# Optimization experiments

Measured on AMD Instinct MI355X. Metric: run time of the kernel, lower is better.

Reference implementation:

```python
import jax, jax.numpy as jnp
import numpy as np

N = 2048; E = 65536; T = 6; F_IN = 2
H_ENC = 256; LAT = 128; H_DEC = 256
PRED = 6
MIN_X, MAX_X = 0.0, 1.0
MIN_Y, MAX_Y = 0.0, 1.0
MIN_EW, MAX_EW = 0.0, 0.5
VISUAL_RANGE = 0.5


def setup_inputs() -> dict:
    key = jax.random.key(0)
    ks = jax.random.split(key, 17)
    p = lambda k, shape: jax.random.normal(k, shape, jnp.float32) * 0.05
    return {
        "x_seq": jax.random.uniform(ks[0], (T, N, F_IN), jnp.float32),
        "edge_index_seq": jax.random.randint(ks[1], (T, 2, E), 0, N),
        "edge_weight_seq": jax.random.uniform(ks[2], (T, E), jnp.float32, 1e-3, 1.0),
        "h_enc": jnp.zeros((N, H_ENC), jnp.float32),
        "h_dec": jnp.zeros((N, H_DEC), jnp.float32),
        "enc_Wx": p(ks[3], (3, 2, F_IN, H_ENC)),
        "enc_bx": p(ks[4], (3, H_ENC)),
        "enc_Wh": p(ks[5], (3, 2, H_ENC, H_ENC)),
        "enc_bh": p(ks[6], (3, H_ENC)),
        "enc_lin_W": p(ks[7], (H_ENC, LAT)),
        "enc_lin_b": p(ks[8], (LAT,)),
        "dec_Wx": p(ks[9], (3, 2, LAT, H_DEC)),
        "dec_bx": p(ks[10], (3, H_DEC)),
        "dec_Wh": p(ks[11], (3, 2, H_DEC, H_DEC)),
        "dec_bh": p(ks[12], (3, H_DEC)),
        "dec_lin_W": p(ks[13], (H_DEC, F_IN)),
        "dec_lin_b": p(ks[14], (F_IN,)),
    }


def _sparse_conv_fn(edge_index, edge_weight, n):
    # ChebConv K=2, sym normalization, lambda_max=2 => T1(L_hat) = -D^-1/2 A D^-1/2
    src, dst = edge_index[0], edge_index[1]
    deg = jax.ops.segment_sum(edge_weight, src, num_segments=n)
    dinv = jnp.where(deg > 0, jax.lax.rsqrt(jnp.where(deg > 0, deg, 1.0)), 0.0)
    norm = -dinv[src] * edge_weight * dinv[dst]  # [E]

    def conv(x, W, b):  # W: [2, in, out]
        tx1 = jax.ops.segment_sum(norm[:, None] * x[src], dst, num_segments=n)
        return x @ W[0] + tx1 @ W[1] + b
    return conv


def _dense_conv_fn(y_hat):
    # graph rebuilt from detached predicted coords (radius graph, dense masked form)
    c = jax.lax.stop_gradient(y_hat)
    px = c[:, 0] * (MAX_X - MIN_X) + MIN_X
    py = c[:, 1] * (MAX_Y - MIN_Y) + MIN_Y
    coords = jnp.stack((px, py), axis=1)  # [N, 2]
    d = jnp.linalg.norm(coords[:, None, :] - coords[None, :, :], axis=2)  # [N, N]
    mask = (d < VISUAL_RANGE) & (d > 0)
    w = jnp.where(mask, (d - MIN_EW) / (MAX_EW - MIN_EW), 0.0)
    deg = w.sum(axis=1)
    dinv = jnp.where(deg > 0, jax.lax.rsqrt(jnp.where(deg > 0, deg, 1.0)), 0.0)
    M = -(dinv[:, None] * w) * dinv[None, :]  # scaled-Laplacian off-diagonal

    def conv(x, W, b):
        return x @ W[0] + (M @ x) @ W[1] + b
    return conv


def _gru(conv, x, H, Wx, bx, Wh, bh):
    # GConvGRU gates: each gate = conv_x(X) + conv_h(H)
    z = jax.nn.sigmoid(conv(x, Wx[0], bx[0]) + conv(H, Wh[0], bh[0]))
    r = jax.nn.sigmoid(conv(x, Wx[1], bx[1]) + conv(H, Wh[1], bh[1]))
    h_tilde = jnp.tanh(conv(x, Wx[2], bx[2]) + conv(H * r, Wh[2], bh[2]))
    return z * H + (1.0 - z) * h_tilde


def reference(x_seq, edge_index_seq, edge_weight_seq, h_enc, h_dec,
              enc_Wx, enc_bx, enc_Wh, enc_bh, enc_lin_W, enc_lin_b,
              dec_Wx, dec_bx, dec_Wh, dec_bh, dec_lin_W, dec_lin_b):
    n = x_seq.shape[1]

    def step(conv, x, he, hd):
        he0 = _gru(conv, x, he, enc_Wx, enc_bx, enc_Wh, enc_bh)
        z = jax.nn.relu(he0) @ enc_lin_W + enc_lin_b
        hd0 = _gru(conv, z, hd, dec_Wx, dec_bx, dec_Wh, dec_bh)
        y_hat = jax.nn.relu(hd0) @ dec_lin_W + dec_lin_b
        return y_hat, he0, hd0

    # observed snapshots (sparse edge-list graphs)
    for t in range(x_seq.shape[0]):
        conv = _sparse_conv_fn(edge_index_seq[t], edge_weight_seq[t], n)
        y_hat, h_enc, h_dec = step(conv, x_seq[t], h_enc, h_dec)

    preds = [y_hat]
    for _ in range(PRED - 1):
        conv = _dense_conv_fn(y_hat)
        y_hat, h_enc, h_dec = step(conv, y_hat, h_enc, h_dec)
        preds.append(y_hat)
    return jnp.stack(preds)  # [PRED, N, 2]
```

## Files before the change

### kernel.cpp

```cpp
#include <hip/hip_runtime.h>
#include <math.h>

#define NN 2048
#define EE 65536
#define T_OBS 6
#define FIN 2
#define HE 256
#define LT 128
#define PREDN 6
#define DMM_NZ 8
#define ZR_NZ 4
#define GT_NZ 8
#define LIN_NZ 8

typedef __attribute__((ext_vector_type(8))) short short8v;
typedef __attribute__((ext_vector_type(4))) float float4v;

static __device__ __forceinline__ unsigned short f2bf(float f) {
    union { float f; unsigned u; } v; v.f = f;
    unsigned r = v.u + 0x7fff + ((v.u >> 16) & 1);
    return (unsigned short)(r >> 16);
}

static __device__ __forceinline__ void bfsplit(float f, unsigned short& h,
                                               unsigned short& l) {
    unsigned u = __float_as_uint(f);
    h = (unsigned short)(u >> 16);
    float hf = __uint_as_float(u & 0xffff0000u);
    l = (unsigned short)(__float_as_uint(f - hf) >> 16);
}

__global__ void k_degcnt(const int* __restrict__ src, const int* __restrict__ dst,
                         const float* __restrict__ ew,
                         float* __restrict__ deg, int* __restrict__ cnt) {
    int e = blockIdx.x * blockDim.x + threadIdx.x;
    if (e < EE) {
        atomicAdd(&deg[src[e]], ew[e]);
        atomicAdd(&cnt[dst[e]], 1);
    }
}

__global__ void k_scan(const int* __restrict__ cnt, const float* __restrict__ deg,
                       int* __restrict__ roff, int* __restrict__ cur,
                       float* __restrict__ dinv) {
    __shared__ int part[256];
    int t = threadIdx.x;
#pragma unroll
    for (int i = t; i < NN; i += 256) {
        float d = deg[i];
        dinv[i] = d > 0.f ? 1.f / sqrtf(d) : 0.f;
    }
    int loc[8];
// ... 15 lines not shown
        roff[idx] = run;
        cur[idx] = run;
        run += loc[i];
    }
    if (t == 255) roff[NN] = run;
}

__global__ void k_scatter2(const int* __restrict__ src, const int* __restrict__ dst,
                           const float* __restrict__ ew, const float* __restrict__ dinv,
                           int* __restrict__ cur,
                           int* __restrict__ csr_src, float* __restrict__ csr_nrm) {
    int e = blockIdx.x * blockDim.x + threadIdx.x;
    if (e < EE) {
        int s = src[e], d = dst[e];
        int p = atomicAdd(&cur[d], 1);
        csr_src[p] = s;
        csr_nrm[p] = -dinv[s] * ew[e] * dinv[d];
    }
}

template <int F>
__global__ void k_spmm_v(const int* __restrict__ roff, const int* __restrict__ csr_src,
                         const float* __restrict__ csr_nrm,
                         const float* __restrict__ X, float* __restrict__ out) {
    int w = threadIdx.x >> 6, lane = threadIdx.x & 63;
    int nid = (blockIdx.x << 2) + w;
    int c = lane << 2;
    int s0 = roff[nid], s1 = roff[nid + 1];
    float4 acc = make_float4(0.f, 0.f, 0.f, 0.f);
    int s = s0;
    for (; s + 8 <= s1; s += 8) {
        int is[8]; float ws[8];
#pragma unroll
        for (int j = 0; j < 8; j++) { is[j] = csr_src[s + j]; ws[j] = csr_nrm[s + j]; }
        if (c < F) {
            float4 xv[8];
#pragma unroll
            for (int j = 0; j < 8; j++) xv[j] = *(const float4*)&X[(size_t)is[j] * F + c];
#pragma unroll
            for (int j = 0; j < 8; j++) {
                acc.x = fmaf(ws[j], xv[j].x, acc.x);
                acc.y = fmaf(ws[j], xv[j].y, acc.y);
                acc.z = fmaf(ws[j], xv[j].z, acc.z);
                acc.w = fmaf(ws[j], xv[j].w, acc.w);
            }
        }
    }
    for (; s < s1; ++s) {
        int i0 = csr_src[s]; float w0 = csr_nrm[s];
        if (c < F) {
            float4 xv = *(const float4*)&X[(size_t)i0 * F + c];
            acc.x = fmaf(w0, xv.x, acc.x);
            acc.y = fmaf(w0, xv.y, acc.y);
            acc.z = fmaf(w0, xv.z, acc.z);
            acc.w = fmaf(w0, xv.w, acc.w);
        }
    }
    if (c < F) *(float4*)&out[(size_t)nid * F + c] = acc;
}

__global__ void k_spmm2(const int* __restrict__ roff, const int* __restrict__ csr_src,
                        const float* __restrict__ csr_nrm,
                        const float* __restrict__ X, float* __restrict__ out) {
    int nid = blockIdx.x * blockDim.x + threadIdx.x;
    if (nid < NN) {
        int s0 = roff[nid], s1 = roff[nid + 1];
        float a0 = 0.f, a1 = 0.f;
        for (int s = s0; s < s1; ++s) {
            int i = csr_src[s]; float w = csr_nrm[s];
            float2 xv = *(const float2*)&X[2 * i];
            a0 = fmaf(w, xv.x, a0);
            a1 = fmaf(w, xv.y, a1);
        }
        out[2 * nid] = a0;
        out[2 * nid + 1] = a1;
    }
}

__global__ void k_ddeg(const float* __restrict__ c, float* __restrict__ dinv) {
    int i = blockIdx.x;
    int t = threadIdx.x;
    float xi = c[2 * i], yi = c[2 * i + 1];
    float s = 0.f;
    for (int j = t; j < NN; j += 256) {
        float dx = xi - c[2 * j], dy = yi - c[2 * j + 1];
        float d = sqrtf(dx * dx + dy * dy);
        if (d > 0.f && d < 0.5f) s += 2.f * d;
    }
    __shared__ float red[256];
    red[t] = s;
    __syncthreads();
    for (int off = 128; off > 0; off >>= 1) {
        if (t < off) red[t] += red[t + off];
        __syncthreads();
    }
    if (t == 0) {
        float d = red[0];
        dinv[i] = d > 0.f ? 1.f / sqrtf(d) : 0.f;
    }
}

__global__ void k_dM(const float* __restrict__ c, const float* __restrict__ dinv,
                     float* __restrict__ M, unsigned short* __restrict__ Mb) {
    int idx = blockIdx.x * blockDim.x + threadIdx.x;
    int i = idx >> 11, j = idx & (NN - 1);
    float dx = c[2 * i] - c[2 * j], dy = c[2 * i + 1] - c[2 * j + 1];
    float d = sqrtf(dx * dx + dy * dy);
    float w = (d > 0.f && d < 0.5f) ? 2.f * d : 0.f;
    float v = -(dinv[i] * w) * dinv[j];
    M[idx] = v;
    Mb[idx] = f2bf(v);
}

template <int F>
__global__ __launch_bounds__(256) void k_dmm_mf(
    const unsigned short* __restrict__ Mb, const float* __restrict__ X,
    float* __restrict__ pbuf)
{
    __shared__ __align__(16) unsigned short Ms[64][72];
    __shared__ __align__(16) unsigned short Xs[64][72];
    const int tid = threadIdx.x;
    const int wid = tid >> 6, lane = tid & 63;
    const int m0 = blockIdx.x << 6, n0 = blockIdx.y << 6;
    const int kb0 = blockIdx.z << 8;
    const int lr = lane & 15;
    const int kg = lane >> 4;
    float4v acc[4];
#pragma unroll
    for (int t = 0; t < 4; t++) acc[t] = (float4v){0.f, 0.f, 0.f, 0.f};

    for (int kb = kb0; kb < kb0 + 256; kb += 64) {
#pragma unroll
        for (int it = 0; it < 2; it++) {
            int i = tid + it * 256;
// ... 21 lines not shown
        __syncthreads();
#pragma unroll
        for (int kh = 0; kh < 2; kh++) {
            int kk = kh * 32 + kg * 8;
            short8v a = *(const short8v*)&Ms[(wid << 4) + lr][kk];
#pragma unroll
            for (int t = 0; t < 4; t++) {
                short8v b = *(const short8v*)&Xs[(t << 4) + lr][kk];
                acc[t] = __builtin_amdgcn_mfma_f32_16x16x32_bf16(a, b, acc[t], 0, 0, 0);
            }
        }
        __syncthreads();
    }
    float* p = pbuf + (size_t)blockIdx.z * NN * F;
#pragma unroll
    for (int t = 0; t < 4; t++)
#pragma unroll
        for (int j = 0; j < 4; j++)
            p[(size_t)(m0 + (wid << 4) + (kg << 2) + j) * F + n0 + (t << 4) + lr] =
                acc[t][j];
}

template <int F, int NZ>
__global__ void k_redks(const float* __restrict__ pbuf, float* __restrict__ out) {
    const int TOT = NN * F / 4;
    int i = blockIdx.x * blockDim.x + threadIdx.x;
    if (i < TOT) {
        const float4* p = (const float4*)pbuf;
        float4 s = p[i];
#pragma unroll
        for (int z = 1; z < NZ; z++) {
            float4 v = p[(size_t)z * TOT + i];
            s.x += v.x; s.y += v.y; s.z += v.z; s.w += v.w;
        }
        ((float4*)out)[i] = s;
    }
}

__global__ void k_dmv2(const float* __restrict__ M, const float* __restrict__ X,
                       float* __restrict__ out) {
    int i = blockIdx.x;
    int t = threadIdx.x;
    float a0 = 0.f, a1 = 0.f;
    for (int j = t; j < NN; j += 256) {
        float m = M[i * NN + j];
        a0 = fmaf(m, X[2 * j], a0);
        a1 = fmaf(m, X[2 * j + 1], a1);
    }
    __shared__ float r0[256], r1[256];
    r0[t] = a0;
    r1[t] = a1;
    __syncthreads();
    for (int off = 128; off > 0; off >>= 1) {
        if (t < off) { r0[t] += r0[t + off]; r1[t] += r1[t + off]; }
        __syncthreads();
    }
    if (t == 0) { out[2 * i] = r0[0]; out[2 * i + 1] = r1[0]; }
}

template <bool RELU>
__device__ __forceinline__ void mfma_seg(
    unsigned short (*Ah)[40], unsigned short (*Al)[40],
    unsigned short (*Bh)[40], unsigned short (*Bl)[40],
    const float* __restrict__ A, int lda,
    const float* __restrict__ B, int ldb, int K,
    int m0, int tid, int wid, int lr, int kg, float4v (&acc)[4])
{
    for (int k0 = 0; k0 < K; k0 += 32) {
        {
            int r = tid >> 2, k8 = (tid & 3) << 3;
            const float* ap = &A[(size_t)(m0 + r) * lda + k0 + k8];
            float4 va = *(const float4*)ap;
            float4 vb = *(const float4*)(ap + 4);
            float v[8] = {va.x, va.y, va.z, va.w, vb.x, vb.y, vb.z, vb.w};
            short8v hv, lv;
#pragma unroll
            for (int j = 0; j < 8; j++) {
                float f = RELU ? fmaxf(v[j], 0.f) : v[j];
                unsigned short h, l;
                bfsplit(f, h, l);
                hv[j] = (short)h; lv[j] = (short)l;
            }
            *(short8v*)&Ah[r][k8] = hv;
            *(short8v*)&Al[r][k8] = lv;
        }
        {
            int k2 = (tid & 15) << 1;
            int n4 = (tid >> 4) << 2;
            const float* bp = &B[(size_t)(k0 + k2) * ldb + n4];
            float4 va = *(const float4*)bp;
            float4 vb = *(const float4*)(bp + ldb);
            float v0[4] = {va.x, va.y, va.z, va.w};
            float v1[4] = {vb.x, vb.y, vb.z, vb.w};
#pragma unroll
            for (int j = 0; j < 4; j++) {
                unsigned short h0, l0, h1, l1;
                bfsplit(v0[j], h0, l0);
                bfsplit(v1[j], h1, l1);
                *(unsigned*)&Bh[n4 + j][k2] = (unsigned)h0 | ((unsigned)h1 << 16);
                *(unsigned*)&Bl[n4 + j][k2] = (unsigned)l0 | ((unsigned)l1 << 16);
            }
        }
        __syncthreads();
        short8v ah = *(short8v*)&Ah[(wid << 4) + lr][kg << 3];
        short8v al = *(short8v*)&Al[(wid << 4) + lr][kg << 3];
#pragma unroll
        for (int t = 0; t < 4; t++) {
            short8v bh = *(short8v*)&Bh[(t << 4) + lr][kg << 3];
            short8v bl = *(short8v*)&Bl[(t << 4) + lr][kg << 3];
            acc[t] = __builtin_amdgcn_mfma_f32_16x16x32_bf16(ah, bh, acc[t], 0, 0, 0);
            acc[t] = __builtin_amdgcn_mfma_f32_16x16x32_bf16(ah, bl, acc[t], 0, 0, 0);
            acc[t] = __builtin_amdgcn_mfma_f32_16x16x32_bf16(al, bh, acc[t], 0, 0, 0);
        }
        __syncthreads();
    }
}

__global__ __launch_bounds__(256) void k_zr_ks(
    const float* __restrict__ A0, int K01, const float* __restrict__ A1,
    const float* __restrict__ H, const float* __restrict__ A3,
    const float* __restrict__ Wx, const float* __restrict__ Wh,
    float* __restrict__ pbuf)
{
    __shared__ __align__(16) unsigned short Ah[64][40], Al[64][40],
                                            Bh[64][40], Bl[64][40];
    int tid = threadIdx.x;
    int wid = tid >> 6, lane = tid & 63, lr = lane & 15, kg = lane >> 4;
    int m0 = blockIdx.x << 6;
    int g = blockIdx.y >> 2;
    int n0 = (blockIdx.y & 3) << 6;
    float4v acc[4];
#pragma unroll
    for (int t = 0; t < 4; t++) acc[t] = (float4v){0.f, 0.f, 0.f, 0.f};
    const float* As[4] = {A0, A1, H, A3};
    const int ldas[4] = {K01, K01, HE, HE};
    const float* Bs[4] = {
        Wx + (size_t)(g * 2 + 0) * K01 * HE + n0,
        Wx + (size_t)(g * 2 + 1) * K01 * HE + n0,
        Wh + (size_t)(g * 2 + 0) * HE * HE + n0,
        Wh + (size_t)(g * 2 + 1) * HE * HE + n0};
    const int Ks[4] = {K01, K01, HE, HE};
    int chunk = (2 * K01 + 2 * HE) / ZR_NZ;
    int lo = blockIdx.z * chunk, hi = lo + chunk;
    int off = 0;
#pragma unroll
    for (int s = 0; s < 4; s++) {
        int a = lo - off; a = a < 0 ? 0 : a;
        int b = hi - off; b = b > Ks[s] ? Ks[s] : b;
        if (b > a)
            mfma_seg<false>(Ah, Al, Bh, Bl, As[s] + a, ldas[s],
                            Bs[s] + (size_t)a * HE, HE, b - a,
                            m0, tid, wid, lr, kg, acc);
        off += Ks[s];
    }
    float* p = pbuf + (size_t)blockIdx.z * NN * 512;
    int cbase = (g << 8) + n0;
#pragma unroll
    for (int t = 0; t < 4; t++)
#pragma unroll
        for (int j = 0; j < 4; j++)
            p[(size_t)(m0 + (wid << 4) + (kg << 2) + j) * 512 + cbase + (t << 4) + lr] =
                acc[t][j];
}

__global__ void k_zr_ep(const float* __restrict__ pbuf,
                        const float* __restrict__ bx, const float* __restrict__ bh,
                        const float* __restrict__ H,
                        const float* __restrict__ x2, const float* __restrict__ ax2,
                        const float* __restrict__ Wx,
                        float* __restrict__ gz, float* __restrict__ hr)
{
    int i = blockIdx.x * 256 + threadIdx.x;
    const float4* p = (const float4*)pbuf;
    const size_t S = (size_t)NN * 512 / 4;
    float4 a = p[i];
#pragma unroll
    for (int z = 1; z < ZR_NZ; z++) {
        float4 v = p[(size_t)z * S + i];
        a.x += v.x; a.y += v.y; a.z += v.z; a.w += v.w;
    }
    int row = i >> 7, c = (i & 127) << 2;
    int g = c >> 8, cc = c & 255;
    if (Wx) {
        float x0 = x2[2 * row], x1 = x2[2 * row + 1];
        float q0 = ax2[2 * row], q1 = ax2[2 * row + 1];
        const float* W0 = Wx + (size_t)(g * 2 + 0) * FIN * HE;
        const float* W1 = Wx + (size_t)(g * 2 + 1) * FIN * HE;
        float4 w00 = *(const float4*)&W0[cc];
        float4 w01 = *(const float4*)&W0[HE + cc];
        float4 w10 = *(const float4*)&W1[cc];
        float4 w11 = *(const float4*)&W1[HE + cc];
        a.x += x0 * w00.x + x1 * w01.x + q0 * w10.x + q1 * w11.x;
        a.y += x0 * w00.y + x1 * w01.y + q0 * w10.y + q1 * w11.y;
        a.z += x0 * w00.z + x1 * w01.z + q0 * w10.z + q1 * w11.z;
        a.w += x0 * w00.w + x1 * w01.w + q0 * w10.w + q1 * w11.w;
    }
    float4 b0 = *(const float4*)&bx[c];
    float4 b1 = *(const float4*)&bh[c];
    float4 s;
    s.x = 1.f / (1.f + expf(-(a.x + b0.x + b1.x)));
    s.y = 1.f / (1.f + expf(-(a.y + b0.y + b1.y)));
    s.z = 1.f / (1.f + expf(-(a.z + b0.z + b1.z)));
    s.w = 1.f / (1.f + expf(-(a.w + b0.w + b1.w)));
    if (c < HE) {
        *(float4*)&gz[(size_t)row * HE + c] = s;
    } else {
        float4 h = *(const float4*)&H[(size_t)row * HE + cc];
        s.x *= h.x; s.y *= h.y; s.z *= h.z; s.w *= h.w;
        *(float4*)&hr[(size_t)row * HE + cc] = s;
    }
}

__global__ __launch_bounds__(256) void k_gt_ks(
    const float* __restrict__ A0, int K01, const float* __restrict__ A1,
    const float* __restrict__ hr, const float* __restrict__ A3,
    const float* __restrict__ Wx2, const float* __restrict__ Wh2,
    float* __restrict__ pbuf)
{
    __shared__ __align__(16) unsigned short Ah[64][40], Al[64][40],
                                            Bh[64][40], Bl[64][40];
    int tid = threadIdx.x;
    int wid = tid >> 6, lane = tid & 63, lr = lane & 15, kg = lane >> 4;
    int m0 = blockIdx.x << 6;
    int n0 = blockIdx.y << 6;
    float4v acc[4];
#pragma unroll
    for (int t = 0; t < 4; t++) acc[t] = (float4v){0.f, 0.f, 0.f, 0.f};
    const float* As[4] = {A0, A1, hr, A3};
    const int ldas[4] = {K01, K01, HE, HE};
    const float* Bs[4] = {
        Wx2 + n0,
        Wx2 + (size_t)K01 * HE + n0,
        Wh2 + n0,
        Wh2 + (size_t)HE * HE + n0};
    const int Ks[4] = {K01, K01, HE, HE};
    int chunk = (2 * K01 + 2 * HE) / GT_NZ;
    int lo = blockIdx.z * chunk, hi = lo + chunk;
    int off = 0;
#pragma unroll
    for (int s = 0; s < 4; s++) {
        int a = lo - off; a = a < 0 ? 0 : a;
        int b = hi - off; b = b > Ks[s] ? Ks[s] : b;
        if (b > a)
            mfma_seg<false>(Ah, Al, Bh, Bl, As[s] + a, ldas[s],
                            Bs[s] + (size_t)a * HE, HE, b - a,
                            m0, tid, wid, lr, kg, acc);
        off += Ks[s];
    }
    float* p = pbuf + (size_t)blockIdx.z * NN * HE;
#pragma unroll
    for (int t = 0; t < 4; t++)
#pragma unroll
        for (int j = 0; j < 4; j++)
            p[(size_t)(m0 + (wid << 4) + (kg << 2) + j) * HE + n0 + (t << 4) + lr] =
                acc[t][j];
}

__global__ void k_gt_ep(const float* __restrict__ pbuf,
                        const float* __restrict__ bx2, const float* __restrict__ bh2,
                        const float* __restrict__ gz,
                        const float* __restrict__ x2, const float* __restrict__ ax2,
                        const float* __restrict__ Wx2,
                        float* __restrict__ H)
{
    int i = blockIdx.x * 256 + threadIdx.x;
    const float4* p = (const float4*)pbuf;
    const size_t S = (size_t)NN * HE / 4;
    float4 a = p[i];
#pragma unroll
    for (int z = 1; z < GT_NZ; z++) {
        float4 v = p[(size_t)z * S + i];
        a.x += v.x; a.y += v.y; a.z += v.z; a.w += v.w;
    }
    int row = i >> 6, c = (i & 63) << 2;
    if (Wx2) {
        float x0 = x2[2 * row], x1 = x2[2 * row + 1];
        float q0 = ax2[2 * row], q1 = ax2[2 * row + 1];
        float4 w00 = *(const float4*)&Wx2[c];
        float4 w01 = *(const float4*)&Wx2[HE + c];
        float4 w10 = *(const float4*)&Wx2[2 * HE + c];
        float4 w11 = *(const float4*)&Wx2[3 * HE + c];
        a.x += x0 * w00.x + x1 * w01.x + q0 * w10.x + q1 * w11.x;
        a.y += x0 * w00.y + x1 * w01.y + q0 * w10.y + q1 * w11.y;
        a.z += x0 * w00.z + x1 * w01.z + q0 * w10.z + q1 * w11.z;
        a.w += x0 * w00.w + x1 * w01.w + q0 * w10.w + q1 * w11.w;
    }
    float4 b0 = *(const float4*)&bx2[c];
    float4 b1 = *(const float4*)&bh2[c];
    size_t idx = (size_t)row * HE + c;
    float4 z = *(const float4*)&gz[idx];
    float4 h = *(const float4*)&H[idx];
    float4 o;
    o.x = z.x * h.x + (1.f - z.x) * tanhf(a.x + b0.x + b1.x);
    o.y = z.y * h.y + (1.f - z.y) * tanhf(a.y + b0.y + b1.y);
    o.z = z.z * h.z + (1.f - z.z) * tanhf(a.z + b0.z + b1.z);
    o.w = z.w * h.w + (1.f - z.w) * tanhf(a.w + b0.w + b1.w);
    *(float4*)&H[idx] = o;
}

__global__ __launch_bounds__(256) void k_lin_ks(
    const float* __restrict__ A, const float* __restrict__ B,
    float* __restrict__ pbuf)
{
    __shared__ __align__(16) unsigned short Ah[64][40], Al[64][40],
                                            Bh[64][40], Bl[64][40];
    int tid = threadIdx.x;
    int wid = tid >> 6, lane = tid & 63, lr = lane & 15, kg = lane >> 4;
    int m0 = blockIdx.x << 6;
    int n0 = blockIdx.y << 6;
    int lo = blockIdx.z << 5;
    float4v acc[4];
#pragma unroll
    for (int t = 0; t < 4; t++) acc[t] = (float4v){0.f, 0.f, 0.f, 0.f};
    mfma_seg<true>(Ah, Al, Bh, Bl, A + lo, HE, B + (size_t)lo * LT + n0, LT, 32,
                   m0, tid, wid, lr, kg, acc);
    float* p = pbuf + (size_t)blockIdx.z * NN * LT;
#pragma unroll
    for (int t = 0; t < 4; t++)
#pragma unroll
        for (int j = 0; j < 4; j++)
            p[(size_t)(m0 + (wid << 4) + (kg << 2) + j) * LT + n0 + (t << 4) + lr] =
                acc[t][j];
}

__global__ void k_lin_ep(const float* __restrict__ pbuf,
                         const float* __restrict__ bias, float* __restrict__ out)
{
    int i = blockIdx.x * 256 + threadIdx.x;
    const float4* p = (const float4*)pbuf;
    const size_t S = (size_t)NN * LT / 4;
    int c = (i & 31) << 2;
    float4 bb = *(const float4*)&bias[c];
    float4 s = make_float4(bb.x, bb.y, bb.z, bb.w);
#pragma unroll
    for (int z = 0; z < LIN_NZ; z++) {
        float4 v = p[z * S + i];
        s.x += v.x; s.y += v.y; s.z += v.z; s.w += v.w;
    }
    ((float4*)out)[i] = s;
}

__global__ void k_declin(const float* __restrict__ A, const float* __restrict__ B,
                         const float* __restrict__ bias, float* __restrict__ out) {
    int w = threadIdx.x >> 6, lane = threadIdx.x & 63;
    int m = blockIdx.x * 4 + w;
    float4 a = *(const float4*)&A[(size_t)m * HE + (lane << 2)];
    float av[4] = {a.x, a.y, a.z, a.w};
    float a0 = 0.f, a1 = 0.f;
#pragma unroll
    for (int j = 0; j < 4; j++) {
        float v = fmaxf(av[j], 0.f);
        float2 b = *(const float2*)&B[((lane << 2) + j) * 2];
        a0 = fmaf(v, b.x, a0);
        a1 = fmaf(v, b.y, a1);
    }
    for (int off = 32; off > 0; off >>= 1) {
        a0 += __shfl_down(a0, off, 64);
        a1 += __shfl_down(a1, off, 64);
    }
    if (lane == 0) {
        out[2 * m] = a0 + bias[0];
        out[2 * m + 1] = a1 + bias[1];
// ... 17 lines not shown
    const float* elinb = (const float*)d_in[10];
    const float* decWx = (const float*)d_in[11];
    const float* decbx = (const float*)d_in[12];
    const float* decWh = (const float*)d_in[13];
    const float* decbh = (const float*)d_in[14];
    const float* dlinW = (const float*)d_in[15];
    const float* dlinb = (const float*)d_in[16];
    float* out = (float*)d_out;

    float* W = (float*)d_ws;
    float* h_enc = W; W += (size_t)NN * HE;
    float* h_dec = W; W += (size_t)NN * HE;
    float* aggx  = W; W += (size_t)NN * HE;
    float* aggh  = W; W += (size_t)NN * HE;
    float* hr    = W; W += (size_t)NN * HE;
    float* agghr = W; W += (size_t)NN * HE;
    float* gz    = W; W += (size_t)NN * HE;
    float* zlat  = W; W += (size_t)NN * LT;
    float* yhat  = W; W += (size_t)NN * FIN;
    float* deg   = W; W += NN;
    int*   cnt   = (int*)W; W += NN;
    float* dinv  = W; W += NN;
    float* csr_nrm = W; W += EE;
    float* Mm    = W; W += (size_t)NN * NN;
    unsigned short* Mb = (unsigned short*)W; W += (size_t)NN * NN / 2;
    float* pbuf  = W; W += (size_t)ZR_NZ * NN * 512;
    int* roff = (int*)W;
    int* cur  = roff + (NN + 2);
    int* csr_src = cur + NN;

    hipMemcpyAsync(h_enc, h_enc_in, sizeof(float) * NN * HE, hipMemcpyDeviceToDevice, stream);
    hipMemcpyAsync(h_dec, h_dec_in, sizeof(float) * NN * HE, hipMemcpyDeviceToDevice, stream);

    for (int step = 0; step < T_OBS + PREDN - 1; ++step) {
        bool sparse = step < T_OBS;
        const float* xin;
        if (sparse) {
            const int* srcp = ei + (size_t)step * 2 * EE;
            const int* dstp = srcp + EE;
            const float* ewt = ews + (size_t)step * EE;
            hipMemsetAsync(deg, 0, sizeof(float) * NN * 2, stream);
            k_degcnt<<<EE / 256, 256, 0, stream>>>(srcp, dstp, ewt, deg, cnt);
            k_scan<<<1, 256, 0, stream>>>(cnt, deg, roff, cur, dinv);
            k_scatter2<<<EE / 256, 256, 0, stream>>>(srcp, dstp, ewt, dinv, cur,
                                                     csr_src, csr_nrm);
            xin = x_seq + (size_t)step * NN * FIN;
        } else {
            k_ddeg<<<NN, 256, 0, stream>>>(yhat, dinv);
            k_dM<<<(NN * NN) / 256, 256, 0, stream>>>(yhat, dinv, Mm, Mb);
            xin = yhat;
        }

        if (sparse) k_spmm2<<<NN / 256, 256, 0, stream>>>(roff, csr_src, csr_nrm, xin, aggx);
        else        k_dmv2<<<NN, 256, 0, stream>>>(Mm, xin, aggx);
        if (sparse) {
            k_spmm_v<HE><<<NN / 4, 256, 0, stream>>>(roff, csr_src, csr_nrm, h_enc, aggh);
        } else {
            k_dmm_mf<HE><<<dim3(NN / 64, HE / 64, DMM_NZ), 256, 0, stream>>>(Mb, h_enc, pbuf);
            k_redks<HE, DMM_NZ><<<NN * HE / 4 / 256, 256, 0, stream>>>(pbuf, aggh);
        }
        k_zr_ks<<<dim3(NN / 64, 8, ZR_NZ), 256, 0, stream>>>(xin, 0, aggx, h_enc, aggh,
                                                             encWx, encWh, pbuf);
        k_zr_ep<<<NN * 512 / 4 / 256, 256, 0, stream>>>(pbuf, encbx, encbh, h_enc,
                                                        xin, aggx, encWx, gz, hr);
        if (sparse) {
            k_spmm_v<HE><<<NN / 4, 256, 0, stream>>>(roff, csr_src, csr_nrm, hr, agghr);
        } else {
            k_dmm_mf<HE><<<dim3(NN / 64, HE / 64, DMM_NZ), 256, 0, stream>>>(Mb, hr, pbuf);
            k_redks<HE, DMM_NZ><<<NN * HE / 4 / 256, 256, 0, stream>>>(pbuf, agghr);
        }
        k_gt_ks<<<dim3(NN / 64, 4, GT_NZ), 256, 0, stream>>>(xin, 0, aggx, hr, agghr,
                                                             encWx + 4 * FIN * HE,
                                                             encWh + 4 * HE * HE, pbuf);
        k_gt_ep<<<NN * HE / 4 / 256, 256, 0, stream>>>(pbuf, encbx + 2 * HE,
                                                       encbh + 2 * HE, gz,
                                                       xin, aggx, encWx + 4 * FIN * HE,
                                                       h_enc);
        k_lin_ks<<<dim3(NN / 64, 2, LIN_NZ), 256, 0, stream>>>(h_enc, elinW, pbuf);
        k_lin_ep<<<NN * LT / 4 / 256, 256, 0, stream>>>(pbuf, elinb, zlat);

        if (sparse) {
            k_spmm_v<LT><<<NN / 4, 256, 0, stream>>>(roff, csr_src, csr_nrm, zlat, aggx);
        } else {
            k_dmm_mf<LT><<<dim3(NN / 64, LT / 64, DMM_NZ), 256, 0, stream>>>(Mb, zlat, pbuf);
            k_redks<LT, DMM_NZ><<<NN * LT / 4 / 256, 256, 0, stream>>>(pbuf, aggx);
        }
        if (sparse) {
            k_spmm_v<HE><<<NN / 4, 256, 0, stream>>>(roff, csr_src, csr_nrm, h_dec, aggh);
        } else {
            k_dmm_mf<HE><<<dim3(NN / 64, HE / 64, DMM_NZ), 256, 0, stream>>>(Mb, h_dec, pbuf);
            k_redks<HE, DMM_NZ><<<NN * HE / 4 / 256, 256, 0, stream>>>(pbuf, aggh);
        }
        k_zr_ks<<<dim3(NN / 64, 8, ZR_NZ), 256, 0, stream>>>(zlat, LT, aggx, h_dec, aggh,
                                                             decWx, decWh, pbuf);
        k_zr_ep<<<NN * 512 / 4 / 256, 256, 0, stream>>>(pbuf, decbx, decbh, h_dec,
                                                        nullptr, nullptr, nullptr, gz, hr);
        if (sparse) {
            k_spmm_v<HE><<<NN / 4, 256, 0, stream>>>(roff, csr_src, csr_nrm, hr, agghr);
        } else {
            k_dmm_mf<HE><<<dim3(NN / 64, HE / 64, DMM_NZ), 256, 0, stream>>>(Mb, hr, pbuf);
            k_redks<HE, DMM_NZ><<<NN * HE / 4 / 256, 256, 0, stream>>>(pbuf, agghr);
        }
        k_gt_ks<<<dim3(NN / 64, 4, GT_NZ), 256, 0, stream>>>(zlat, LT, aggx, hr, agghr,
                                                             decWx + 4 * LT * HE,
                                                             decWh + 4 * HE * HE, pbuf);
        k_gt_ep<<<NN * HE / 4 / 256, 256, 0, stream>>>(pbuf, decbx + 2 * HE,
                                                       decbh + 2 * HE, gz,
                                                       nullptr, nullptr, nullptr,
                                                       h_dec);
        k_declin<<<NN / 4, 256, 0, stream>>>(h_dec, dlinW, dlinb, yhat);

        if (step >= T_OBS - 1) {
            hipMemcpyAsync(out + (size_t)(step - (T_OBS - 1)) * NN * FIN, yhat,
                           sizeof(float) * NN * FIN, hipMemcpyDeviceToDevice, stream);
        }
    }
}
```

Measured before the change: 1.983 ms.

## Pre-split activations and transposed weights into bf16 hi/lo buffers for MFMA GEMMs

```diff
diff --git a/kernel.cpp b/kernel.cpp
--- a/kernel.cpp
+++ b/kernel.cpp
@@ -14,6 +14,7 @@
 #define LIN_NZ 8
 
 typedef __attribute__((ext_vector_type(8))) short short8v;
+typedef __attribute__((ext_vector_type(4))) short short4v;
 typedef __attribute__((ext_vector_type(4))) float float4v;
 
 static __device__ __forceinline__ unsigned short f2bf(float f) {
@@ -28,6 +29,43 @@
     h = (unsigned short)(u >> 16);
     float hf = __uint_as_float(u & 0xffff0000u);
     l = (unsigned short)(__float_as_uint(f - hf) >> 16);
+}
+
+static __device__ __forceinline__ void split4(float4 v, short4v& h, short4v& l) {
+    unsigned short hh, ll;
+    bfsplit(v.x, hh, ll); h[0] = (short)hh; l[0] = (short)ll;
+    bfsplit(v.y, hh, ll); h[1] = (short)hh; l[1] = (short)ll;
+    bfsplit(v.z, hh, ll); h[2] = (short)hh; l[2] = (short)ll;
+    bfsplit(v.w, hh, ll); h[3] = (short)hh; l[3] = (short)ll;
+}
+
+static __device__ __forceinline__ float bf2f(unsigned short b) {
+    return __uint_as_float(((unsigned)b) << 16);
+}
+
+__global__ void k_tsplit(const float* __restrict__ in, unsigned short* __restrict__ oh,
+                         unsigned short* __restrict__ ol, int K, int N) {
+    size_t base = (size_t)blockIdx.y * K * N;
+    int idx = blockIdx.x * 256 + threadIdx.x;
+    if (idx < K * N) {
+        int k = idx / N, n = idx - k * N;
+        unsigned short h, l;
+        bfsplit(in[base + idx], h, l);
+        oh[base + (size_t)n * K + k] = h;
+        ol[base + (size_t)n * K + k] = l;
+    }
+}
+
+__global__ void k_cvt(const float* __restrict__ in, unsigned short* __restrict__ oh,
+                      unsigned short* __restrict__ ol, int n4) {
+    int i = blockIdx.x * 256 + threadIdx.x;
+    if (i < n4) {
+        float4 v = ((const float4*)in)[i];
+        short4v h, l;
+        split4(v, h, l);
+        *(short4v*)&oh[(size_t)i * 4] = h;
+        *(short4v*)&ol[(size_t)i * 4] = l;
+    }
 }
 
 __global__ void k_degcnt(const int* __restrict__ src, const int* __restrict__ dst,
@@ -89,7 +127,8 @@
 template <int F>
 __global__ void k_spmm_v(const int* __restrict__ roff, const int* __restrict__ csr_src,
                          const float* __restrict__ csr_nrm,
-                         const float* __restrict__ X, float* __restrict__ out) {
+                         const float* __restrict__ X, float* __restrict__ out,
+                         unsigned short* __restrict__ oh, unsigned short* __restrict__ ol) {
     int w = threadIdx.x >> 6, lane = threadIdx.x & 63;
     int nid = (blockIdx.x << 2) + w;
     int c = lane << 2;
@@ -123,7 +162,13 @@
             acc.w = fmaf(w0, xv.w, acc.w);
         }
     }
-    if (c < F) *(float4*)&out[(size_t)nid * F + c] = acc;
+    if (c < F) {
+        *(float4*)&out[(size_t)nid * F + c] = acc;
+        short4v h, l;
+        split4(acc, h, l);
+        *(short4v*)&oh[(size_t)nid * F + c] = h;
+        *(short4v*)&ol[(size_t)nid * F + c] = l;
+    }
 }
 
 __global__ void k_spmm2(const int* __restrict__ roff, const int* __restrict__ csr_src,
@@ -168,15 +213,13 @@
 }
 
 __global__ void k_dM(const float* __restrict__ c, const float* __restrict__ dinv,
-                     float* __restrict__ M, unsigned short* __restrict__ Mb) {
+                     unsigned short* __restrict__ Mb) {
     int idx = blockIdx.x * blockDim.x + threadIdx.x;
     int i = idx >> 11, j = idx & (NN - 1);
     float dx = c[2 * i] - c[2 * j], dy = c[2 * i + 1] - c[2 * j + 1];
     float d = sqrtf(dx * dx + dy * dy);
     float w = (d > 0.f && d < 0.5f) ? 2.f * d : 0.f;
-    float v = -(dinv[i] * w) * dinv[j];
-    M[idx] = v;
-    Mb[idx] = f2bf(v);
+    Mb[idx] = f2bf(-(dinv[i] * w) * dinv[j]);
 }
 
 template <int F>
@@ -244,7 +287,8 @@
 }
 
 template <int F, int NZ>
-__global__ void k_redks(const float* __restrict__ pbuf, float* __restrict__ out) {
+__global__ void k_redks(const float* __restrict__ pbuf, float* __restrict__ out,
+                        unsigned short* __restrict__ oh, unsigned short* __restrict__ ol) {
     const int TOT = NN * F / 4;
     int i = blockIdx.x * blockDim.x + threadIdx.x;
     if (i < TOT) {
@@ -256,16 +300,20 @@
             s.x += v.x; s.y += v.y; s.z += v.z; s.w += v.w;
         }
         ((float4*)out)[i] = s;
-    }
-}
-
-__global__ void k_dmv2(const float* __restrict__ M, const float* __restrict__ X,
-                       float* __restrict__ out) {
+        short4v h, l;
+        split4(s, h, l);
+        *(short4v*)&oh[(size_t)i * 4] = h;
+        *(short4v*)&ol[(size_t)i * 4] = l;
+    }
+}
+
+__global__ void k_dmv2b(const unsigned short* __restrict__ Mb, const float* __restrict__ X,
+                        float* __restrict__ out) {
     int i = blockIdx.x;
     int t = threadIdx.x;
     float a0 = 0.f, a1 = 0.f;
     for (int j = t; j < NN; j += 256) {
-        float m = M[i * NN + j];
+        float m = bf2f(Mb[(size_t)i * NN + j]);
         a0 = fmaf(m, X[2 * j], a0);
         a1 = fmaf(m, X[2 * j + 1], a1);
     }
@@ -280,68 +328,15 @@
     if (t == 0) { out[2 * i] = r0[0]; out[2 * i + 1] = r1[0]; }
 }
 
-template <bool RELU>
-__device__ __forceinline__ void mfma_seg(
-    unsigned short (*Ah)[40], unsigned short (*Al)[40],
-    unsigned short (*Bh)[40], unsigned short (*Bl)[40],
-    const float* __restrict__ A, int lda,
-    const float* __restrict__ B, int ldb, int K,
-    int m0, int tid, int wid, int lr, int kg, float4v (&acc)[4])
-{
-    for (int k0 = 0; k0 < K; k0 += 32) {
-        {
-            int r = tid >> 2, k8 = (tid & 3) << 3;
-            const float* ap = &A[(size_t)(m0 + r) * lda + k0 + k8];
-            float4 va = *(const float4*)ap;
-            float4 vb = *(const float4*)(ap + 4);
-            float v[8] = {va.x, va.y, va.z, va.w, vb.x, vb.y, vb.z, vb.w};
-            short8v hv, lv;
-#pragma unroll
-            for (int j = 0; j < 8; j++) {
-                float f = RELU ? fmaxf(v[j], 0.f) : v[j];
-                unsigned short h, l;
-                bfsplit(f, h, l);
-                hv[j] = (short)h; lv[j] = (short)l;
-            }
-            *(short8v*)&Ah[r][k8] = hv;
-            *(short8v*)&Al[r][k8] = lv;
-        }
-        {
-            int k2 = (tid & 15) << 1;
-            int n4 = (tid >> 4) << 2;
-            const float* bp = &B[(size_t)(k0 + k2) * ldb + n4];
-            float4 va = *(const float4*)bp;
-            float4 vb = *(const float4*)(bp + ldb);
-            float v0[4] = {va.x, va.y, va.z, va.w};
-            float v1[4] = {vb.x, vb.y, vb.z, vb.w};
-#pragma unroll
-            for (int j = 0; j < 4; j++) {
-                unsigned short h0, l0, h1, l1;
-                bfsplit(v0[j], h0, l0);
-                bfsplit(v1[j], h1, l1);
-                *(unsigned*)&Bh[n4 + j][k2] = (unsigned)h0 | ((unsigned)h1 << 16);
-                *(unsigned*)&Bl[n4 + j][k2] = (unsigned)l0 | ((unsigned)l1 << 16);
-            }
-        }
-        __syncthreads();
-        short8v ah = *(short8v*)&Ah[(wid << 4) + lr][kg << 3];
-        short8v al = *(short8v*)&Al[(wid << 4) + lr][kg << 3];
-#pragma unroll
-        for (int t = 0; t < 4; t++) {
-            short8v bh = *(short8v*)&Bh[(t << 4) + lr][kg << 3];
-            short8v bl = *(short8v*)&Bl[(t << 4) + lr][kg << 3];
-            acc[t] = __builtin_amdgcn_mfma_f32_16x16x32_bf16(ah, bh, acc[t], 0, 0, 0);
-            acc[t] = __builtin_amdgcn_mfma_f32_16x16x32_bf16(ah, bl, acc[t], 0, 0, 0);
-            acc[t] = __builtin_amdgcn_mfma_f32_16x16x32_bf16(al, bh, acc[t], 0, 0, 0);
-        }
-        __syncthreads();
-    }
-}
-
-__global__ __launch_bounds__(256) void k_zr_ks(
-    const float* __restrict__ A0, int K01, const float* __restrict__ A1,
-    const float* __restrict__ H, const float* __restrict__ A3,
-    const float* __restrict__ Wx, const float* __restrict__ Wh,
+struct Seg {
+    const unsigned short* ah; const unsigned short* al;
+    const unsigned short* bh; const unsigned short* bl;
+    int lda, ldk, K; size_t gstride;
+};
+struct Seg4 { Seg s[4]; };
+
+__global__ __launch_bounds__(256) void k_mf_ks(
+    Seg4 segs, int nseg, int totK, int nz, int useG, int ldp,
     float* __restrict__ pbuf)
 {
     __shared__ __align__(16) unsigned short Ah[64][40], Al[64][40],
@@ -349,39 +344,54 @@
     int tid = threadIdx.x;
     int wid = tid >> 6, lane = tid & 63, lr = lane & 15, kg = lane >> 4;
     int m0 = blockIdx.x << 6;
-    int g = blockIdx.y >> 2;
-    int n0 = (blockIdx.y & 3) << 6;
+    int g = useG ? (int)(blockIdx.y >> 2) : 0;
+    int n0 = useG ? (int)((blockIdx.y & 3) << 6) : (int)(blockIdx.y << 6);
     float4v acc[4];
 #pragma unroll
     for (int t = 0; t < 4; t++) acc[t] = (float4v){0.f, 0.f, 0.f, 0.f};
-    const float* As[4] = {A0, A1, H, A3};
-    const int ldas[4] = {K01, K01, HE, HE};
-    const float* Bs[4] = {
-        Wx + (size_t)(g * 2 + 0) * K01 * HE + n0,
-        Wx + (size_t)(g * 2 + 1) * K01 * HE + n0,
-        Wh + (size_t)(g * 2 + 0) * HE * HE + n0,
-        Wh + (size_t)(g * 2 + 1) * HE * HE + n0};
-    const int Ks[4] = {K01, K01, HE, HE};
-    int chunk = (2 * K01 + 2 * HE) / ZR_NZ;
+    int chunk = totK / nz;
     int lo = blockIdx.z * chunk, hi = lo + chunk;
     int off = 0;
-#pragma unroll
-    for (int s = 0; s < 4; s++) {
-        int a = lo - off; a = a < 0 ? 0 : a;
-        int b = hi - off; b = b > Ks[s] ? Ks[s] : b;
-        if (b > a)
-            mfma_seg<false>(Ah, Al, Bh, Bl, As[s] + a, ldas[s],
-                            Bs[s] + (size_t)a * HE, HE, b - a,
-                            m0, tid, wid, lr, kg, acc);
-        off += Ks[s];
-    }
-    float* p = pbuf + (size_t)blockIdx.z * NN * 512;
-    int cbase = (g << 8) + n0;
+    int r = tid >> 2, k8 = (tid & 3) << 3;
+    for (int s = 0; s < nseg; s++) {
+        Seg sg = segs.s[s];
+        int a = lo - off; if (a < 0) a = 0;
+        int b = hi - off; if (b > sg.K) b = sg.K;
+        if (b > a) {
+            const unsigned short* bhp = sg.bh + (size_t)g * sg.gstride;
+            const unsigned short* blp = sg.bl + (size_t)g * sg.gstride;
+            for (int k0 = a; k0 < b; k0 += 32) {
+                *(short8v*)&Ah[r][k8] =
+                    *(const short8v*)&sg.ah[(size_t)(m0 + r) * sg.lda + k0 + k8];
+                *(short8v*)&Al[r][k8] =
+                    *(const short8v*)&sg.al[(size_t)(m0 + r) * sg.lda + k0 + k8];
+                *(short8v*)&Bh[r][k8] =
+                    *(const short8v*)&bhp[(size_t)(n0 + r) * sg.ldk + k0 + k8];
+                *(short8v*)&Bl[r][k8] =
+                    *(const short8v*)&blp[(size_t)(n0 + r) * sg.ldk + k0 + k8];
+                __syncthreads();
+                short8v ahv = *(short8v*)&Ah[(wid << 4) + lr][kg << 3];
+                short8v alv = *(short8v*)&Al[(wid << 4) + lr][kg << 3];
+#pragma unroll
+                for (int t = 0; t < 4; t++) {
+                    short8v bhv = *(short8v*)&Bh[(t << 4) + lr][kg << 3];
+                    short8v blv = *(short8v*)&Bl[(t << 4) + lr][kg << 3];
+                    acc[t] = __builtin_amdgcn_mfma_f32_16x16x32_bf16(ahv, bhv, acc[t], 0, 0, 0);
+                    acc[t] = __builtin_amdgcn_mfma_f32_16x16x32_bf16(ahv, blv, acc[t], 0, 0, 0);
+                    acc[t] = __builtin_amdgcn_mfma_f32_16x16x32_bf16(alv, bhv, acc[t], 0, 0, 0);
+                }
+                __syncthreads();
+            }
+        }
+        off += sg.K;
+    }
+    float* p = pbuf + (size_t)blockIdx.z * NN * ldp;
+    int cbase = (useG ? (g << 8) : 0) + n0;
 #pragma unroll
     for (int t = 0; t < 4; t++)
 #pragma unroll
         for (int j = 0; j < 4; j++)
-            p[(size_t)(m0 + (wid << 4) + (kg << 2) + j) * 512 + cbase + (t << 4) + lr] =
+            p[(size_t)(m0 + (wid << 4) + (kg << 2) + j) * ldp + cbase + (t << 4) + lr] =
                 acc[t][j];
 }
 
@@ -390,7 +400,8 @@
                         const float* __restrict__ H,
                         const float* __restrict__ x2, const float* __restrict__ ax2,
                         const float* __restrict__ Wx,
-                        float* __restrict__ gz, float* __restrict__ hr)
+                        float* __restrict__ gz, float* __restrict__ hr,
+                        unsigned short* __restrict__ hrh, unsigned short* __restrict__ hrl)
 {
     int i = blockIdx.x * 256 + threadIdx.x;
     const float4* p = (const float4*)pbuf;
@@ -427,55 +438,15 @@
     if (c < HE) {
         *(float4*)&gz[(size_t)row * HE + c] = s;
     } else {
-        float4 h = *(const float4*)&H[(size_t)row * HE + cc];
+        size_t idx = (size_t)row * HE + cc;
+        float4 h = *(const float4*)&H[idx];
         s.x *= h.x; s.y *= h.y; s.z *= h.z; s.w *= h.w;
-        *(float4*)&hr[(size_t)row * HE + cc] = s;
-    }
-}
-
-__global__ __launch_bounds__(256) void k_gt_ks(
-    const float* __restrict__ A0, int K01, const float* __restrict__ A1,
-    const float* __restrict__ hr, const float* __restrict__ A3,
-    const float* __restrict__ Wx2, const float* __restrict__ Wh2,
-    float* __restrict__ pbuf)
-{
-    __shared__ __align__(16) unsigned short Ah[64][40], Al[64][40],
-                                            Bh[64][40], Bl[64][40];
-    int tid = threadIdx.x;
-    int wid = tid >> 6, lane = tid & 63, lr = lane & 15, kg = lane >> 4;
-    int m0 = blockIdx.x << 6;
-    int n0 = blockIdx.y << 6;
-    float4v acc[4];
-#pragma unroll
-    for (int t = 0; t < 4; t++) acc[t] = (float4v){0.f, 0.f, 0.f, 0.f};
-    const float* As[4] = {A0, A1, hr, A3};
-    const int ldas[4] = {K01, K01, HE, HE};
-    const float* Bs[4] = {
-        Wx2 + n0,
-        Wx2 + (size_t)K01 * HE + n0,
-        Wh2 + n0,
-        Wh2 + (size_t)HE * HE + n0};
-    const int Ks[4] = {K01, K01, HE, HE};
-    int chunk = (2 * K01 + 2 * HE) / GT_NZ;
-    int lo = blockIdx.z * chunk, hi = lo + chunk;
-    int off = 0;
-#pragma unroll
-    for (int s = 0; s < 4; s++) {
-        int a = lo - off; a = a < 0 ? 0 : a;
-        int b = hi - off; b = b > Ks[s] ? Ks[s] : b;
-        if (b > a)
-            mfma_seg<false>(Ah, Al, Bh, Bl, As[s] + a, ldas[s],
-                            Bs[s] + (size_t)a * HE, HE, b - a,
-                            m0, tid, wid, lr, kg, acc);
-        off += Ks[s];
-    }
-    float* p = pbuf + (size_t)blockIdx.z * NN * HE;
-#pragma unroll
-    for (int t = 0; t < 4; t++)
-#pragma unroll
-        for (int j = 0; j < 4; j++)
-            p[(size_t)(m0 + (wid << 4) + (kg << 2) + j) * HE + n0 + (t << 4) + lr] =
-                acc[t][j];
+        *(float4*)&hr[idx] = s;
+        short4v sh, sl;
+        split4(s, sh, sl);
+        *(short4v*)&hrh[idx] = sh;
+        *(short4v*)&hrl[idx] = sl;
+    }
 }
 
 __global__ void k_gt_ep(const float* __restrict__ pbuf,
@@ -483,7 +454,9 @@
                         const float* __restrict__ gz,
                         const float* __restrict__ x2, const float* __restrict__ ax2,
                         const float* __restrict__ Wx2,
-                        float* __restrict__ H)
+                        float* __restrict__ H,
+                        unsigned short* __restrict__ Hh, unsigned short* __restrict__ Hl,
+                        unsigned short* __restrict__ rhh, unsigned short* __restrict__ rhl)
 {
     int i = blockIdx.x * 256 + threadIdx.x;
     const float4* p = (const float4*)pbuf;
@@ -518,35 +491,23 @@
     o.z = z.z * h.z + (1.f - z.z) * tanhf(a.z + b0.z + b1.z);
     o.w = z.w * h.w + (1.f - z.w) * tanhf(a.w + b0.w + b1.w);
     *(float4*)&H[idx] = o;
-}
-
-__global__ __launch_bounds__(256) void k_lin_ks(
-    const float* __restrict__ A, const float* __restrict__ B,
-    float* __restrict__ pbuf)
-{
-    __shared__ __align__(16) unsigned short Ah[64][40], Al[64][40],
-                                            Bh[64][40], Bl[64][40];
-    int tid = threadIdx.x;
-    int wid = tid >> 6, lane = tid & 63, lr = lane & 15, kg = lane >> 4;
-    int m0 = blockIdx.x << 6;
-    int n0 = blockIdx.y << 6;
-    int lo = blockIdx.z << 5;
-    float4v acc[4];
-#pragma unroll
-    for (int t = 0; t < 4; t++) acc[t] = (float4v){0.f, 0.f, 0.f, 0.f};
-    mfma_seg<true>(Ah, Al, Bh, Bl, A + lo, HE, B + (size_t)lo * LT + n0, LT, 32,
-                   m0, tid, wid, lr, kg, acc);
-    float* p = pbuf + (size_t)blockIdx.z * NN * LT;
-#pragma unroll
-    for (int t = 0; t < 4; t++)
-#pragma unroll
-        for (int j = 0; j < 4; j++)
-            p[(size_t)(m0 + (wid << 4) + (kg << 2) + j) * LT + n0 + (t << 4) + lr] =
-                acc[t][j];
+    short4v sh, sl;
+    split4(o, sh, sl);
+    *(short4v*)&Hh[idx] = sh;
+    *(short4v*)&Hl[idx] = sl;
+    if (rhh) {
+        float4 rr;
+        rr.x = fmaxf(o.x, 0.f); rr.y = fmaxf(o.y, 0.f);
+        rr.z = fmaxf(o.z, 0.f); rr.w = fmaxf(o.w, 0.f);
+        split4(rr, sh, sl);
+        *(short4v*)&rhh[idx] = sh;
+        *(short4v*)&rhl[idx] = sl;
+    }
 }
 
 __global__ void k_lin_ep(const float* __restrict__ pbuf,
-                         const float* __restrict__ bias, float* __restrict__ out)
+                         const float* __restrict__ bias, float* __restrict__ out,
+                         unsigned short* __restrict__ oh, unsigned short* __restrict__ ol)
 {
     int i = blockIdx.x * 256 + threadIdx.x;
     const float4* p = (const float4*)pbuf;
@@ -560,6 +521,10 @@
         s.x += v.x; s.y += v.y; s.z += v.z; s.w += v.w;
     }
     ((float4*)out)[i] = s;
+    short4v sh, sl;
+    split4(s, sh, sl);
+    *(short4v*)&oh[(size_t)i * 4] = sh;
+    *(short4v*)&ol[(size_t)i * 4] = sl;
 }
 
 __global__ void k_declin(const float* __restrict__ A, const float* __restrict__ B,
@@ -623,15 +588,47 @@
     int*   cnt   = (int*)W; W += NN;
     float* dinv  = W; W += NN;
     float* csr_nrm = W; W += EE;
-    float* Mm    = W; W += (size_t)NN * NN;
     unsigned short* Mb = (unsigned short*)W; W += (size_t)NN * NN / 2;
     float* pbuf  = W; W += (size_t)ZR_NZ * NN * 512;
+    unsigned short* HenH = (unsigned short*)W; W += (size_t)NN * HE / 2;
+    unsigned short* HenL = (unsigned short*)W; W += (size_t)NN * HE / 2;
+    unsigned short* HdeH = (unsigned short*)W; W += (size_t)NN * HE / 2;
+    unsigned short* HdeL = (unsigned short*)W; W += (size_t)NN * HE / 2;
+    unsigned short* agghH = (unsigned short*)W; W += (size_t)NN * HE / 2;
+    unsigned short* agghL = (unsigned short*)W; W += (size_t)NN * HE / 2;
+    unsigned short* agghrH = (unsigned short*)W; W += (size_t)NN * HE / 2;
+    unsigned short* agghrL = (unsigned short*)W; W += (size_t)NN * HE / 2;
+    unsigned short* hrH = (unsigned short*)W; W += (size_t)NN * HE / 2;
+    unsigned short* hrL = (unsigned short*)W; W += (size_t)NN * HE / 2;
+    unsigned short* rhH = (unsigned short*)W; W += (size_t)NN * HE / 2;
+    unsigned short* rhL = (unsigned short*)W; W += (size_t)NN * HE / 2;
+    unsigned short* zlatH = (unsigned short*)W; W += (size_t)NN * LT / 2;
+    unsigned short* zlatL = (unsigned short*)W; W += (size_t)NN * LT / 2;
+    unsigned short* aggxdH = (unsigned short*)W; W += (size_t)NN * LT / 2;
+    unsigned short* aggxdL = (unsigned short*)W; W += (size_t)NN * LT / 2;
+    unsigned short* WehT_h = (unsigned short*)W; W += (size_t)6 * HE * HE / 2;
+    unsigned short* WehT_l = (unsigned short*)W; W += (size_t)6 * HE * HE / 2;
+    unsigned short* WdhT_h = (unsigned short*)W; W += (size_t)6 * HE * HE / 2;
+    unsigned short* WdhT_l = (unsigned short*)W; W += (size_t)6 * HE * HE / 2;
+    unsigned short* WdxT_h = (unsigned short*)W; W += (size_t)6 * HE * LT / 2;
+    unsigned short* WdxT_l = (unsigned short*)W; W += (size_t)6 * HE * LT / 2;
+    unsigned short* elinT_h = (unsigned short*)W; W += (size_t)HE * LT / 2;
+    unsigned short* elinT_l = (unsigned short*)W; W += (size_t)HE * LT / 2;
     int* roff = (int*)W;
     int* cur  = roff + (NN + 2);
     int* csr_src = cur + NN;
 
+    k_tsplit<<<dim3(HE * HE / 256, 6), 256, 0, stream>>>(encWh, WehT_h, WehT_l, HE, HE);
+    k_tsplit<<<dim3(HE * HE / 256, 6), 256, 0, stream>>>(decWh, WdhT_h, WdhT_l, HE, HE);
+    k_tsplit<<<dim3(LT * HE / 256, 6), 256, 0, stream>>>(decWx, WdxT_h, WdxT_l, LT, HE);
+    k_tsplit<<<dim3(HE * LT / 256, 1), 256, 0, stream>>>(elinW, elinT_h, elinT_l, HE, LT);
+    k_cvt<<<NN * HE / 4 / 256, 256, 0, stream>>>(h_enc_in, HenH, HenL, NN * HE / 4);
+    k_cvt<<<NN * HE / 4 / 256, 256, 0, stream>>>(h_dec_in, HdeH, HdeL, NN * HE / 4);
     hipMemcpyAsync(h_enc, h_enc_in, sizeof(float) * NN * HE, hipMemcpyDeviceToDevice, stream);
     hipMemcpyAsync(h_dec, h_dec_in, sizeof(float) * NN * HE, hipMemcpyDeviceToDevice, stream);
+
+    const size_t WH = (size_t)HE * HE;
+    const size_t WX = (size_t)HE * LT;
 
     for (int step = 0; step < T_OBS + PREDN - 1; ++step) {
         bool sparse = step < T_OBS;
@@ -648,67 +645,93 @@
             xin = x_seq + (size_t)step * NN * FIN;
         } else {
             k_ddeg<<<NN, 256, 0, stream>>>(yhat, dinv);
-            k_dM<<<(NN * NN) / 256, 256, 0, stream>>>(yhat, dinv, Mm, Mb);
+            k_dM<<<(NN * NN) / 256, 256, 0, stream>>>(yhat, dinv, Mb);
             xin = yhat;
         }
 
         if (sparse) k_spmm2<<<NN / 256, 256, 0, stream>>>(roff, csr_src, csr_nrm, xin, aggx);
-        else        k_dmv2<<<NN, 256, 0, stream>>>(Mm, xin, aggx);
+        else        k_dmv2b<<<NN, 256, 0, stream>>>(Mb, xin, aggx);
         if (sparse) {
-            k_spmm_v<HE><<<NN / 4, 256, 0, stream>>>(roff, csr_src, csr_nrm, h_enc, aggh);
+            k_spmm_v<HE><<<NN / 4, 256, 0, stream>>>(roff, csr_src, csr_nrm, h_enc,
+                                                     aggh, agghH, agghL);
         } else {
             k_dmm_mf<HE><<<dim3(NN / 64, HE / 64, DMM_NZ), 256, 0, stream>>>(Mb, h_enc, pbuf);
-            k_redks<HE, DMM_NZ><<<NN * HE / 4 / 256, 256, 0, stream>>>(pbuf, aggh);
-        }
-        k_zr_ks<<<dim3(NN / 64, 8, ZR_NZ), 256, 0, stream>>>(xin, 0, aggx, h_enc, aggh,
-                                                             encWx, encWh, pbuf);
+            k_redks<HE, DMM_NZ><<<NN * HE / 4 / 256, 256, 0, stream>>>(pbuf, aggh, agghH, agghL);
+        }
+        {
+            Seg4 sg = {};
+            sg.s[0] = {HenH, HenL, WehT_h, WehT_l, HE, HE, HE, 2 * WH};
+            sg.s[1] = {agghH, agghL, WehT_h + WH, WehT_l + WH, HE, HE, HE, 2 * WH};
+            k_mf_ks<<<dim3(NN / 64, 8, ZR_NZ), 256, 0, stream>>>(sg, 2, 512, ZR_NZ, 1, 512, pbuf);
+        }
         k_zr_ep<<<NN * 512 / 4 / 256, 256, 0, stream>>>(pbuf, encbx, encbh, h_enc,
-                                                        xin, aggx, encWx, gz, hr);
+                                                        xin, aggx, encWx, gz, hr, hrH, hrL);
         if (sparse) {
-            k_spmm_v<HE><<<NN / 4, 256, 0, stream>>>(roff, csr_src, csr_nrm, hr, agghr);
+            k_spmm_v<HE><<<NN / 4, 256, 0, stream>>>(roff, csr_src, csr_nrm, hr,
+                                                     agghr, agghrH, agghrL);
         } else {
             k_dmm_mf<HE><<<dim3(NN / 64, HE / 64, DMM_NZ), 256, 0, stream>>>(Mb, hr, pbuf);
-            k_redks<HE, DMM_NZ><<<NN * HE / 4 / 256, 256, 0, stream>>>(pbuf, agghr);
-        }
-        k_gt_ks<<<dim3(NN / 64, 4, GT_NZ), 256, 0, stream>>>(xin, 0, aggx, hr, agghr,
-                                                             encWx + 4 * FIN * HE,
-                                                             encWh + 4 * HE * HE, pbuf);
-        k_gt_ep<<<NN * HE / 4 / 256, 256, 0, stream>>>(pbuf, encbx + 2 * HE,
-                                                       encbh + 2 * HE, gz,
-                                                       xin, aggx, encWx + 4 * FIN * HE,
-                                                       h_enc);
-        k_lin_ks<<<dim3(NN / 64, 2, LIN_NZ), 256, 0, stream>>>(h_enc, elinW, pbuf);
-        k_lin_ep<<<NN * LT / 4 / 256, 256, 0, stream>>>(pbuf, elinb, zlat);
+            k_redks<HE, DMM_NZ><<<NN * HE / 4 / 256, 256, 0, stream>>>(pbuf, agghr, agghrH, agghrL);
+        }
+        {
+            Seg4 sg = {};
+            sg.s[0] = {hrH, hrL, WehT_h + 4 * WH, WehT_l + 4 * WH, HE, HE, HE, 0};
+            sg.s[1] = {agghrH, agghrL, WehT_h + 5 * WH, WehT_l + 5 * WH, HE, HE, HE, 0};
+            k_mf_ks<<<dim3(NN / 64, 4, GT_NZ), 256, 0, stream>>>(sg, 2, 512, GT_NZ, 0, HE, pbuf);
+        }
+        k_gt_ep<<<NN * HE / 4 / 256, 256, 0, stream>>>(pbuf, encbx + 2 * HE, encbh + 2 * HE,
+                                                       gz, xin, aggx, encWx + 4 * FIN * HE,
+                                                       h_enc, HenH, HenL, rhH, rhL);
+        {
+            Seg4 sg = {};
+            sg.s[0] = {rhH, rhL, elinT_h, elinT_l, HE, HE, HE, 0};
+            k_mf_ks<<<dim3(NN / 64, 2, LIN_NZ), 256, 0, stream>>>(sg, 1, 256, LIN_NZ, 0, LT, pbuf);
+        }
+        k_lin_ep<<<NN * LT / 4 / 256, 256, 0, stream>>>(pbuf, elinb, zlat, zlatH, zlatL);
 
         if (sparse) {
-            k_spmm_v<LT><<<NN / 4, 256, 0, stream>>>(roff, csr_src, csr_nrm, zlat, aggx);
+            k_spmm_v<LT><<<NN / 4, 256, 0, stream>>>(roff, csr_src, csr_nrm, zlat,
+                                                     aggx, aggxdH, aggxdL);
         } else {
             k_dmm_mf<LT><<<dim3(NN / 64, LT / 64, DMM_NZ), 256, 0, stream>>>(Mb, zlat, pbuf);
-            k_redks<LT, DMM_NZ><<<NN * LT / 4 / 256, 256, 0, stream>>>(pbuf, aggx);
+            k_redks<LT, DMM_NZ><<<NN * LT / 4 / 256, 256, 0, stream>>>(pbuf, aggx, aggxdH, aggxdL);
         }
         if (sparse) {
-            k_spmm_v<HE><<<NN / 4, 256, 0, stream>>>(roff, csr_src, csr_nrm, h_dec, aggh);
+            k_spmm_v<HE><<<NN / 4, 256, 0, stream>>>(roff, csr_src, csr_nrm, h_dec,
+                                                     aggh, agghH, agghL);
         } else {
             k_dmm_mf<HE><<<dim3(NN / 64, HE / 64, DMM_NZ), 256, 0, stream>>>(Mb, h_dec, pbuf);
-            k_redks<HE, DMM_NZ><<<NN * HE / 4 / 256, 256, 0, stream>>>(pbuf, aggh);
-        }
-        k_zr_ks<<<dim3(NN / 64, 8, ZR_NZ), 256, 0, stream>>>(zlat, LT, aggx, h_dec, aggh,
-                                                             decWx, decWh, pbuf);
+            k_redks<HE, DMM_NZ><<<NN * HE / 4 / 256, 256, 0, stream>>>(pbuf, aggh, agghH, agghL);
+        }
+        {
+            Seg4 sg = {};
+            sg.s[0] = {zlatH, zlatL, WdxT_h, WdxT_l, LT, LT, LT, 2 * WX};
+            sg.s[1] = {aggxdH, aggxdL, WdxT_h + WX, WdxT_l + WX, LT, LT, LT, 2 * WX};
+            sg.s[2] = {HdeH, HdeL, WdhT_h, WdhT_l, HE, HE, HE, 2 * WH};
+            sg.s[3] = {agghH, agghL, WdhT_h + WH, WdhT_l + WH, HE, HE, HE, 2 * WH};
+            k_mf_ks<<<dim3(NN / 64, 8, ZR_NZ), 256, 0, stream>>>(sg, 4, 768, ZR_NZ, 1, 512, pbuf);
+        }
         k_zr_ep<<<NN * 512 / 4 / 256, 256, 0, stream>>>(pbuf, decbx, decbh, h_dec,
-                                                        nullptr, nullptr, nullptr, gz, hr);
+                                                        nullptr, nullptr, nullptr,
+                                                        gz, hr, hrH, hrL);
         if (sparse) {
-            k_spmm_v<HE><<<NN / 4, 256, 0, stream>>>(roff, csr_src, csr_nrm, hr, agghr);
+            k_spmm_v<HE><<<NN / 4, 256, 0, stream>>>(roff, csr_src, csr_nrm, hr,
+                                                     agghr, agghrH, agghrL);
         } else {
             k_dmm_mf<HE><<<dim3(NN / 64, HE / 64, DMM_NZ), 256, 0, stream>>>(Mb, hr, pbuf);
-            k_redks<HE, DMM_NZ><<<NN * HE / 4 / 256, 256, 0, stream>>>(pbuf, agghr);
-        }
-        k_gt_ks<<<dim3(NN / 64, 4, GT_NZ), 256, 0, stream>>>(zlat, LT, aggx, hr, agghr,
-                                                             decWx + 4 * LT * HE,
-                                                             decWh + 4 * HE * HE, pbuf);
-        k_gt_ep<<<NN * HE / 4 / 256, 256, 0, stream>>>(pbuf, decbx + 2 * HE,
-                                                       decbh + 2 * HE, gz,
-                                                       nullptr, nullptr, nullptr,
-                                                       h_dec);
+            k_redks<HE, DMM_NZ><<<NN * HE / 4 / 256, 256, 0, stream>>>(pbuf, agghr, agghrH, agghrL);
+        }
+        {
+            Seg4 sg = {};
+            sg.s[0] = {zlatH, zlatL, WdxT_h + 4 * WX, WdxT_l + 4 * WX, LT, LT, LT, 0};
+            sg.s[1] = {aggxdH, aggxdL, WdxT_h + 5 * WX, WdxT_l + 5 * WX, LT, LT, LT, 0};
+            sg.s[2] = {hrH, hrL, WdhT_h + 4 * WH, WdhT_l + 4 * WH, HE, HE, HE, 0};
+            sg.s[3] = {agghrH, agghrL, WdhT_h + 5 * WH, WdhT_l + 5 * WH, HE, HE, HE, 0};
+            k_mf_ks<<<dim3(NN / 64, 4, GT_NZ), 256, 0, stream>>>(sg, 4, 768, GT_NZ, 0, HE, pbuf);
+        }
+        k_gt_ep<<<NN * HE / 4 / 256, 256, 0, stream>>>(pbuf, decbx + 2 * HE, decbh + 2 * HE,
+                                                       gz, nullptr, nullptr, nullptr,
+                                                       h_dec, HdeH, HdeL, nullptr, nullptr);
         k_declin<<<NN / 4, 256, 0, stream>>>(h_dec, dlinW, dlinb, yhat);
 
         if (step >= T_OBS - 1) {
```

After: 2.057 ms. 1.04x slower.
